# Kernel tuning notes

Measured on AMD Instinct MI355X. Metric: run time of the kernel, lower is better.

The kernel has to match this reference:

```python
import jax, jax.numpy as jnp
import numpy as np

B, N, DEG, RATIO = 100, 1000, 16, 0.8
E = B * N * DEG                      # 1.6M edges
K1 = int(np.ceil(RATIO * N))         # 800
K2 = int(np.ceil(RATIO * K1))        # 640
K3 = int(np.ceil(RATIO * K2))        # 512
F_IN, H, OUT = 128, 128, 10


def _graph_conv(x, src, dst, emask, w_root, w_rel, b):
    # PyG GraphConv (aggr='add'): out = lin_rel(sum_j x_j) + lin_root(x) + bias
    msg = x[src] * emask[:, None].astype(x.dtype)               # [E, F]
    agg = jax.ops.segment_sum(msg, dst, num_segments=x.shape[0])
    return agg @ w_rel.T + x @ w_root.T + b


def _topk_pool(x, src, dst, emask, w, n_per_graph, k):
    # PyG TopKPooling: score = tanh((x.w)/||w||); keep top-k per graph; x *= score
    score = jnp.tanh((x @ w) / jnp.linalg.norm(w))              # [B*n]
    vals, idx = jax.lax.top_k(score.reshape(B, n_per_graph), k)  # [B,k]
    perm = (idx + jnp.arange(B)[:, None] * n_per_graph).reshape(-1)
    new_x = x[perm] * vals.reshape(-1, 1)
    mapping = jnp.full(B * n_per_graph, -1, dtype=jnp.int32).at[perm].set(
        jnp.arange(B * k, dtype=jnp.int32))
    ns, nd = mapping[src], mapping[dst]
    valid = emask & (ns >= 0) & (nd >= 0)
    return new_x, jnp.where(valid, ns, 0), jnp.where(valid, nd, 0), valid


def _global_pool(x, k):
    xg = x.reshape(B, k, x.shape[-1])
    return jnp.concatenate([xg.max(axis=1), xg.mean(axis=1)], axis=1)  # [B, 2H]


def setup_inputs() -> dict:
    key = jax.random.key(0)
    ks = jax.random.split(key, 16)
    x = jax.random.normal(ks[0], (B * N, F_IN), jnp.float32)
    src = jax.random.randint(ks[1], (B, N * DEG), 0, N)
    dst = jax.random.randint(ks[2], (B, N * DEG), 0, N)
    off = (jnp.arange(B) * N)[:, None]
    edge_index = jnp.stack([(src + off).reshape(-1), (dst + off).reshape(-1)])

    def lin(k, fo, fi):
        return jax.random.normal(k, (fo, fi), jnp.float32) / np.sqrt(fi).astype(np.float32)

    return {
        'x': x, 'edge_index': edge_index,
        'w_root1': lin(ks[3], H, F_IN), 'w_rel1': lin(ks[4], H, F_IN), 'b1': jnp.zeros((H,), jnp.float32),
        'pw1': jax.random.normal(ks[5], (H,), jnp.float32),
        'w_root2': lin(ks[6], H, H), 'w_rel2': lin(ks[7], H, H), 'b2': jnp.zeros((H,), jnp.float32),
        'pw2': jax.random.normal(ks[8], (H,), jnp.float32),
        'w_root3': lin(ks[9], H, H), 'w_rel3': lin(ks[10], H, H), 'b3': jnp.zeros((H,), jnp.float32),
        'pw3': jax.random.normal(ks[11], (H,), jnp.float32),
        'lin1_w': lin(ks[12], 128, 256), 'lin1_b': jnp.zeros((128,), jnp.float32),
        'lin2_w': lin(ks[13], 64, 128), 'lin2_b': jnp.zeros((64,), jnp.float32),
        'lin3_w': lin(ks[14], OUT, 64), 'lin3_b': jnp.zeros((OUT,), jnp.float32),
    }


def reference(x, edge_index, w_root1, w_rel1, b1, pw1, w_root2, w_rel2, b2, pw2,
              w_root3, w_rel3, b3, pw3, lin1_w, lin1_b, lin2_w, lin2_b, lin3_w, lin3_b):
    src, dst = edge_index[0], edge_index[1]
    emask = jnp.ones(src.shape[0], dtype=bool)

    h = jax.nn.relu(_graph_conv(x, src, dst, emask, w_root1, w_rel1, b1))
    h, src, dst, emask = _topk_pool(h, src, dst, emask, pw1, N, K1)
    x1 = _global_pool(h, K1)

    h = jax.nn.relu(_graph_conv(h, src, dst, emask, w_root2, w_rel2, b2))
    h, src, dst, emask = _topk_pool(h, src, dst, emask, pw2, K1, K2)
    x2 = _global_pool(h, K2)

    h = jax.nn.relu(_graph_conv(h, src, dst, emask, w_root3, w_rel3, b3))
    h, src, dst, emask = _topk_pool(h, src, dst, emask, pw3, K2, K3)
    x3 = _global_pool(h, K3)

    g = x1 + x2 + x3                                   # [B, 256]
    g = jax.nn.relu(g @ lin1_w.T + lin1_b)             # dropout: eval mode (identity)
    g = jax.nn.relu(g @ lin2_w.T + lin2_b)
    return jax.nn.log_softmax(g @ lin3_w.T + lin3_b, axis=-1)
```

## Files before the change

kernel.cpp:

```cpp
#include <hip/hip_runtime.h>
#include <math.h>

constexpr int BG = 100;
constexpr int NN = 1000;
constexpr int EE = 1600000;
constexpr int NV = 100000;
constexpr int FD = 128;
constexpr int K1 = 800, K2 = 640, K3 = 512;

__device__ __forceinline__ float xla_tanh(float x) {
    const float kClamp = 7.90531110763549805f;
    const float a1 = 4.89352455891786e-03f, a3 = 6.37261928875436e-04f,
                a5 = 1.48572235717979e-05f, a7 = 5.12229709037114e-08f,
                a9 = -8.60467152213735e-11f, a11 = 2.00018790482477e-13f,
                a13 = -2.76076847742355e-16f;
    const float b0 = 4.89352518554385e-03f, b2 = 2.26843463243900e-03f,
                b4 = 1.18534705686654e-04f, b6 = 1.19825839466702e-06f;
    if (fabsf(x) < 4e-04f) return x;
    float xc = fminf(fmaxf(x, -kClamp), kClamp);
    float x2 = xc * xc;
    float p = fmaf(x2, a13, a11);
    p = fmaf(x2, p, a9);
    p = fmaf(x2, p, a7);
    p = fmaf(x2, p, a5);
    p = fmaf(x2, p, a3);
    p = fmaf(x2, p, a1);
    p = xc * p;
    float q = fmaf(x2, b6, b4);
    q = fmaf(x2, q, b2);
    q = fmaf(x2, q, b0);
    return p / q;
}

__global__ __launch_bounds__(256) void zero_k(int* __restrict__ p, int n) {
    int i = blockIdx.x * 256 + threadIdx.x;
    if (i < n) p[i] = 0;
}
__global__ __launch_bounds__(256) void count_k(const int* __restrict__ dst,
                                               int* __restrict__ cnt) {
    int e = blockIdx.x * 256 + threadIdx.x;
    if (e < EE) atomicAdd(&cnt[dst[e]], 1);
}
__global__ __launch_bounds__(1024) void scan1_k(const int* __restrict__ cnt,
                                                int* __restrict__ excl,
                                                int* __restrict__ bsum, int n) {
    __shared__ int s[1024];
    int b = blockIdx.x, t = threadIdx.x, i = b * 1024 + t;
    int v = (i < n) ? cnt[i] : 0;
    s[t] = v; __syncthreads();
    for (int off = 1; off < 1024; off <<= 1) {
        int x = (t >= off) ? s[t - off] : 0;
        __syncthreads();
        s[t] += x;
        __syncthreads();
    }
    if (i < n) excl[i] = s[t] - v;
    if (t == 1023) bsum[b] = s[t];
}
__global__ void scan2_k(int* __restrict__ bsum, int nb) {
    if (threadIdx.x == 0) {
        int acc = 0;
        for (int b = 0; b < nb; ++b) { int v = bsum[b]; bsum[b] = acc; acc += v; }
    }
}
__global__ __launch_bounds__(256) void scan3_k(int* __restrict__ rowptr,
                                               const int* __restrict__ bsum,
                                               int* __restrict__ cursor, int n) {
    int i = blockIdx.x * 256 + threadIdx.x;
    if (i < n) {
        int v = rowptr[i] + bsum[i >> 10];
        rowptr[i] = v;
        cursor[i] = v;
    }
    if (i == 0) rowptr[n] = EE;
}
__global__ __launch_bounds__(256) void fill_k(const int* __restrict__ dst,
                                              int* __restrict__ cursor,
                                              int* __restrict__ eidx) {
    int e = blockIdx.x * 256 + threadIdx.x;
    if (e < EE) {
        int p = atomicAdd(&cursor[dst[e]], 1);
        eidx[p] = e;
    }
}
__global__ __launch_bounds__(256) void compose_k(const int* __restrict__ m1,
                                                 const int* __restrict__ m2,
                                                 int* __restrict__ cm, int n) {
    int i = blockIdx.x * 256 + threadIdx.x;
    if (i < n) { int v = m1[i]; cm[i] = (v < 0) ? -1 : m2[v]; }
}

__global__ __launch_bounds__(128) void gather3_k(
    const float* __restrict__ feat, const int* __restrict__ src,
    const int* __restrict__ rowptr, const int* __restrict__ eidx,
    const int* __restrict__ map, float* __restrict__ agg)
{
    __shared__ int sS[128];
    __shared__ double sred[4][32][4];
    int bid = blockIdx.x;
    int d = (bid & 7) * (NV / 8) + (bid >> 3);
    int t = threadIdx.x;
    int slot = t >> 5;
    int fg   = t & 31;
    int dm = d;
    if (map) { dm = map[d]; if (dm < 0) return; }
    int beg = rowptr[d], end = rowptr[d + 1];
    double a0 = 0.0, a1 = 0.0, a2 = 0.0, a3 = 0.0;
    while (beg < end) {
        int chunk = min(128, end - beg);
        if (t < chunk) {
            int s = src[eidx[beg + t]];
            if (map) s = map[s];
            sS[t] = s;
        }
        __syncthreads();
        for (int i = slot; i < chunk; i += 4) {
            int s = sS[i];
            if (s >= 0) {
                float4 v = *(const float4*)(feat + (size_t)s * FD + fg * 4);
                a0 += (double)v.x; a1 += (double)v.y;
                a2 += (double)v.z; a3 += (double)v.w;
            }
        }
        __syncthreads();
        beg += chunk;
    }
    sred[slot][fg][0] = a0; sred[slot][fg][1] = a1;
    sred[slot][fg][2] = a2; sred[slot][fg][3] = a3;
    __syncthreads();
    if (slot == 0) {
        double r0 = sred[0][fg][0] + sred[1][fg][0] + sred[2][fg][0] + sred[3][fg][0];
        double r1 = sred[0][fg][1] + sred[1][fg][1] + sred[2][fg][1] + sred[3][fg][1];
        double r2 = sred[0][fg][2] + sred[1][fg][2] + sred[2][fg][2] + sred[3][fg][2];
        double r3 = sred[0][fg][3] + sred[1][fg][3] + sred[2][fg][3] + sred[3][fg][3];
        *(float4*)(agg + (size_t)dm * FD + fg * 4) =
            make_float4((float)r0, (float)r1, (float)r2, (float)r3);
    }
}

constexpr int TRR = 32;
constexpr int KS = 64;
constexpr int LDK2 = 68;
__global__ __launch_bounds__(128) void conv_mm4(
    const float* __restrict__ in, float* __restrict__ agg,
    const float* __restrict__ w_root, const float* __restrict__ w_rel,
    const float* __restrict__ bias)
{
    __shared__ float sA[TRR][LDK2];
    __shared__ float sI[TRR][LDK2];
    int r0 = blockIdx.x * TRR;
    int t = threadIdx.x;
    int g  = t >> 6;
    int cp = t & 63;
    const float* wr0 = w_rel  + (size_t)(2 * cp) * FD;
    const float* wr1 = wr0 + FD;
    const float* wo0 = w_root + (size_t)(2 * cp) * FD;
    const float* wo1 = wo0 + FD;
    float acc[2][16];
    #pragma unroll
    for (int c = 0; c < 2; ++c)
        #pragma unroll
        for (int r = 0; r < 16; ++r) acc[c][r] = 0.f;

    #pragma unroll
    for (int ph = 0; ph < 2; ++ph) {
        int kb = ph * KS;
        if (ph) __syncthreads();
        #pragma unroll
        for (int q = 0; q < 8; ++q) {
            int idx = q * 128 + t;
            int row = (idx >> 4) & 31;
            int c4  = idx & 15;
            if (idx < 512) {
                float4 va = *(const float4*)(agg + (size_t)(r0 + row) * FD + kb + c4 * 4);
                *(float4*)&sA[row][c4 * 4] = va;
            } else {
                float4 vi = *(const float4*)(in + (size_t)(r0 + row) * FD + kb + c4 * 4);
                *(float4*)&sI[row][c4 * 4] = vi;
            }
        }
        __syncthreads();
        for (int k0 = kb; k0 < kb + KS; k0 += 4) {
            float4 r0v = *(const float4*)(wr0 + k0);
            float4 r1v = *(const float4*)(wr1 + k0);
            float4 o0v = *(const float4*)(wo0 + k0);
            float4 o1v = *(const float4*)(wo1 + k0);
            int kl = k0 - kb;
            #pragma unroll
            for (int r = 0; r < 16; ++r) {
                float4 a = *(const float4*)&sA[g * 16 + r][kl];
                float4 b = *(const float4*)&sI[g * 16 + r][kl];
                acc[0][r] += a.x * r0v.x + b.x * o0v.x;
                acc[0][r] += a.y * r0v.y + b.y * o0v.y;
                acc[0][r] += a.z * r0v.z + b.z * o0v.z;
                acc[0][r] += a.w * r0v.w + b.w * o0v.w;
                acc[1][r] += a.x * r1v.x + b.x * o1v.x;
                acc[1][r] += a.y * r1v.y + b.y * o1v.y;
                acc[1][r] += a.z * r1v.z + b.z * o1v.z;
                acc[1][r] += a.w * r1v.w + b.w * o1v.w;
            }
        }
    }
    float b0 = bias[2 * cp], b1 = bias[2 * cp + 1];
    #pragma unroll
    for (int r = 0; r < 16; ++r) {
        float v0 = b0 + acc[0][r];
        float v1 = b1 + acc[1][r];
        v0 = v0 > 0.f ? v0 : 0.f;
        v1 = v1 > 0.f ? v1 : 0.f;
        *(float2*)(agg + (size_t)(r0 + g * 16 + r) * FD + 2 * cp) =
            make_float2(v0, v1);
    }
}

__global__ __launch_bounds__(128) void norm_k(const float* __restrict__ pw,
                                              float* __restrict__ nrm)
{
    int t = threadIdx.x;
    float v = pw[t]; v *= v;
    #pragma unroll
    for (int off = 32; off; off >>= 1) v += __shfl_down(v, off);
    __shared__ float s[2];
    if ((t & 63) == 0) s[t >> 6] = v;
    __syncthreads();
    if (t == 0) nrm[0] = sqrtf(s[0] + s[1]);
}

__global__ __launch_bounds__(256) void scores_k(
    const float* __restrict__ h, const float* __restrict__ pw,
    const float* __restrict__ nrm, float* __restrict__ out, int rows)
{
    int gid = blockIdx.x * 256 + threadIdx.x;
    int node = gid >> 6, lane = gid & 63;
    if (node >= rows) return;
    float2 hv = *(const float2*)(h + (size_t)node * FD + lane * 2);
    float2 wv = *(const float2*)(pw + lane * 2);
    double d = (double)hv.x * (double)wv.x + (double)hv.y * (double)wv.y;
    #pragma unroll
    for (int off = 32; off; off >>= 1) d += __shfl_down(d, off);
    if (lane == 0) {
        float arg = (float)d / nrm[0];
        out[node] = xla_tanh(arg);
    }
}

__global__ __launch_bounds__(512) void topk_k(
    const float* __restrict__ h, const float* __restrict__ scores,
    float* __restrict__ outx, int* __restrict__ mapping, int n_per, int k)
{
    __shared__ unsigned long long sk[1024];
    __shared__ int sel[1024];
    int b = blockIdx.x, tid = threadIdx.x;
    for (int i = tid; i < 1024; i += 512) {
        float f = (i < n_per) ? scores[b * n_per + i] : -INFINITY;
        unsigned u = __float_as_uint(f);
        u = (u & 0x80000000u) ? ~u : (u | 0x80000000u);
        sk[i] = ((unsigned long long)u << 32) | (unsigned)(1023 - i);
        sel[i] = -1;
    }
    __syncthreads();
    for (int ksz = 2; ksz <= 1024; ksz <<= 1) {
        for (int j = ksz >> 1; j; j >>= 1) {
            int i = ((tid & ~(j - 1)) << 1) | (tid & (j - 1));
            int p = i | j;
            bool up = ((i & ksz) == 0);
            unsigned long long ki = sk[i], kp = sk[p];
            if ((ki < kp) == up) { sk[i] = kp; sk[p] = ki; }
            __syncthreads();
        }
    }
    for (int i = tid; i < k; i += 512)
        sel[1023 - (unsigned)(sk[i] & 0xFFFFFFFFu)] = i;
    __syncthreads();
    for (int i = tid; i < n_per; i += 512)
        mapping[b * n_per + i] = (sel[i] >= 0) ? b * k + sel[i] : -1;
    for (int t = tid; t < k * 32; t += 512) {
        int nj = t >> 5, f4 = t & 31;
        unsigned long long kk = sk[nj];
        int old = 1023 - (unsigned)(kk & 0xFFFFFFFFu);
        unsigned u = (unsigned)(kk >> 32);
        float val = (u & 0x80000000u) ? __uint_as_float(u & 0x7FFFFFFFu)
                                      : __uint_as_float(~u);
        float4 v = *(const float4*)(h + (size_t)(b * n_per + old) * FD + f4 * 4);
        v.x *= val; v.y *= val; v.z *= val; v.w *= val;
        *(float4*)(outx + (size_t)(b * k + nj) * FD + f4 * 4) = v;
    }
}

__global__ __launch_bounds__(1024) void gpool2_k(const float* __restrict__ xp,
                                                 float* __restrict__ g, int k)
{
    __shared__ float smx[8][128];
    __shared__ float ssm[8][128];
    int b = blockIdx.x, t = threadIdx.x;
    int rg = t >> 7;
    int f  = t & 127;
    float mx = -INFINITY, sm = 0.f;
    for (int j = rg; j < k; j += 8) {
        float v = xp[(size_t)(b * k + j) * FD + f];
        mx = fmaxf(mx, v);
        sm += v;
    }
    smx[rg][f] = mx;
    ssm[rg][f] = sm;
    __syncthreads();
    if (rg == 0) {
        float m = smx[0][f], s = ssm[0][f];
        #pragma unroll
        for (int q = 1; q < 8; ++q) { m = fmaxf(m, smx[q][f]); s += ssm[q][f]; }
        g[b * 256 + f]       += m;
        g[b * 256 + 128 + f] += s * (1.0f / k);
    }
}

__global__ __launch_bounds__(256) void mlp_k(
    const float* __restrict__ g,
    const float* __restrict__ l1w, const float* __restrict__ l1b,
    const float* __restrict__ l2w, const float* __restrict__ l2b,
    const float* __restrict__ l3w, const float* __restrict__ l3b,
    float* __restrict__ out)
{
    __shared__ float s0[256], s1[128], s2[64], s3[10];
    int b = blockIdx.x, t = threadIdx.x;
    s0[t] = g[b * 256 + t];
    __syncthreads();
    if (t < 128) {
        float a = l1b[t];
        for (int kk = 0; kk < 256; ++kk) a += s0[kk] * l1w[t * 256 + kk];
        s1[t] = a > 0.f ? a : 0.f;
    }
    __syncthreads();
    if (t < 64) {
        float a = l2b[t];
        for (int kk = 0; kk < 128; ++kk) a += s1[kk] * l2w[t * 128 + kk];
        s2[t] = a > 0.f ? a : 0.f;
    }
    __syncthreads();
    if (t < 10) {
        float a = l3b[t];
        for (int kk = 0; kk < 64; ++kk) a += s2[kk] * l3w[t * 64 + kk];
        s3[t] = a;
    }
    __syncthreads();
    if (t == 0) {
        float m = s3[0];
        for (int i = 1; i < 10; ++i) m = fmaxf(m, s3[i]);
        float se = 0.f;
        for (int i = 0; i < 10; ++i) se += expf(s3[i] - m);
        float lse = m + logf(se);
        for (int i = 0; i < 10; ++i) out[b * 10 + i] = s3[i] - lse;
    }
}

extern "C" void kernel_launch(void* const* d_in, const int* in_sizes, int n_in,
                              void* d_out, int out_size, void* d_ws, size_t ws_size,
                              hipStream_t stream)
{
    const float* x       = (const float*)d_in[0];
    const int*   ei      = (const int*)d_in[1];
    const int*   src     = ei;
    const int*   dst     = ei + EE;
    const float* w_root1 = (const float*)d_in[2];
    const float* w_rel1  = (const float*)d_in[3];
    const float* b1      = (const float*)d_in[4];
    const float* pw1     = (const float*)d_in[5];
    const float* w_root2 = (const float*)d_in[6];
    const float* w_rel2  = (const float*)d_in[7];
    const float* b2      = (const float*)d_in[8];
    const float* pw2     = (const float*)d_in[9];
    const float* w_root3 = (const float*)d_in[10];
    const float* w_rel3  = (const float*)d_in[11];
    const float* b3      = (const float*)d_in[12];
    const float* pw3     = (const float*)d_in[13];
    const float* l1w     = (const float*)d_in[14];
    const float* l1b     = (const float*)d_in[15];
    const float* l2w     = (const float*)d_in[16];
    const float* l2b     = (const float*)d_in[17];
    const float* l3w     = (const float*)d_in[18];
    const float* l3b     = (const float*)d_in[19];
    float* out = (float*)d_out;

    float* A      = (float*)d_ws;
    float* Bf     = A + (size_t)NV * FD;
    float* scores = Bf + (size_t)80000 * FD;
    float* g      = scores + NV;
    float* nrm    = g + BG * 256;
    int*   map1   = (int*)(nrm + 64);
    int*   map2   = map1 + NV;
    int*   map3   = map2 + 80000;
    int*   rowptr = map3 + 64000;
    int*   cursor = rowptr + NV + 2;
    int*   bsum   = cursor + NV;
    int*   eidx   = bsum + 128;
    int*   cmap   = eidx + EE;

    const int NB_E = (EE + 255) / 256;
    const int NB_V = (NV + 255) / 256;
    const int NB_S = (NV + 1023) / 1024;

    zero_k<<<NB_V, 256, 0, stream>>>(cursor, NV);
    count_k<<<NB_E, 256, 0, stream>>>(dst, cursor);
    scan1_k<<<NB_S, 1024, 0, stream>>>(cursor, rowptr, bsum, NV);
    scan2_k<<<1, 64, 0, stream>>>(bsum, NB_S);
    scan3_k<<<NB_V, 256, 0, stream>>>(rowptr, bsum, cursor, NV);
    fill_k<<<NB_E, 256, 0, stream>>>(dst, cursor, eidx);

    hipMemsetAsync(g, 0, (size_t)BG * 256 * sizeof(float), stream);

    gather3_k<<<NV, 128, 0, stream>>>(x, src, rowptr, eidx, nullptr, A);
    conv_mm4<<<NV / TRR, 128, 0, stream>>>(x, A, w_root1, w_rel1, b1);
    norm_k<<<1, 128, 0, stream>>>(pw1, nrm);
    scores_k<<<NV / 4, 256, 0, stream>>>(A, pw1, nrm, scores, NV);
    topk_k<<<BG, 512, 0, stream>>>(A, scores, Bf, map1, NN, K1);
    gpool2_k<<<BG, 1024, 0, stream>>>(Bf, g, K1);

    gather3_k<<<NV, 128, 0, stream>>>(Bf, src, rowptr, eidx, map1, A);
    conv_mm4<<<(BG * K1) / TRR, 128, 0, stream>>>(Bf, A, w_root2, w_rel2, b2);
    norm_k<<<1, 128, 0, stream>>>(pw2, nrm);
    scores_k<<<(BG * K1) / 4, 256, 0, stream>>>(A, pw2, nrm, scores, BG * K1);
    topk_k<<<BG, 512, 0, stream>>>(A, scores, Bf, map2, K1, K2);
    gpool2_k<<<BG, 1024, 0, stream>>>(Bf, g, K2);

    compose_k<<<NB_V, 256, 0, stream>>>(map1, map2, cmap, NV);
    gather3_k<<<NV, 128, 0, stream>>>(Bf, src, rowptr, eidx, cmap, A);
    conv_mm4<<<(BG * K2) / TRR, 128, 0, stream>>>(Bf, A, w_root3, w_rel3, b3);
    norm_k<<<1, 128, 0, stream>>>(pw3, nrm);
    scores_k<<<(BG * K2) / 4, 256, 0, stream>>>(A, pw3, nrm, scores, BG * K2);
    topk_k<<<BG, 512, 0, stream>>>(A, scores, Bf, map3, K2, K3);
    gpool2_k<<<BG, 1024, 0, stream>>>(Bf, g, K3);

    mlp_k<<<BG, 256, 0, stream>>>(g, l1w, l1b, l2w, l2b, l3w, l3b, out);
}
```

Measured before the change: 922.6 us.

## Store source indices in CSR order and remap them in place per pooling level

```diff
diff --git a/kernel.cpp b/kernel.cpp
--- a/kernel.cpp
+++ b/kernel.cpp
@@ -75,13 +75,19 @@
     if (i == 0) rowptr[n] = EE;
 }
 __global__ __launch_bounds__(256) void fill_k(const int* __restrict__ dst,
+                                              const int* __restrict__ src,
                                               int* __restrict__ cursor,
-                                              int* __restrict__ eidx) {
+                                              int* __restrict__ msrc) {
     int e = blockIdx.x * 256 + threadIdx.x;
     if (e < EE) {
         int p = atomicAdd(&cursor[dst[e]], 1);
-        eidx[p] = e;
-    }
+        msrc[p] = src[e];
+    }
+}
+__global__ __launch_bounds__(256) void remap_k(const int* __restrict__ map,
+                                               int* __restrict__ msrc) {
+    int i = blockIdx.x * 256 + threadIdx.x;
+    if (i < EE) { int v = msrc[i]; msrc[i] = (v < 0) ? -1 : map[v]; }
 }
 __global__ __launch_bounds__(256) void compose_k(const int* __restrict__ m1,
                                                  const int* __restrict__ m2,
@@ -90,12 +96,11 @@
     if (i < n) { int v = m1[i]; cm[i] = (v < 0) ? -1 : m2[v]; }
 }
 
-__global__ __launch_bounds__(128) void gather3_k(
-    const float* __restrict__ feat, const int* __restrict__ src,
-    const int* __restrict__ rowptr, const int* __restrict__ eidx,
-    const int* __restrict__ map, float* __restrict__ agg)
-{
-    __shared__ int sS[128];
+__global__ __launch_bounds__(128) void gather5_k(
+    const float* __restrict__ feat, const int* __restrict__ rowptr,
+    const int* __restrict__ msrc, const int* __restrict__ map,
+    float* __restrict__ agg)
+{
     __shared__ double sred[4][32][4];
     int bid = blockIdx.x;
     int d = (bid & 7) * (NV / 8) + (bid >> 3);
@@ -106,24 +111,13 @@
     if (map) { dm = map[d]; if (dm < 0) return; }
     int beg = rowptr[d], end = rowptr[d + 1];
     double a0 = 0.0, a1 = 0.0, a2 = 0.0, a3 = 0.0;
-    while (beg < end) {
-        int chunk = min(128, end - beg);
-        if (t < chunk) {
-            int s = src[eidx[beg + t]];
-            if (map) s = map[s];
-            sS[t] = s;
+    for (int i = beg + slot; i < end; i += 4) {
+        int s = msrc[i];
+        if (s >= 0) {
+            float4 v = *(const float4*)(feat + (size_t)s * FD + fg * 4);
+            a0 += (double)v.x; a1 += (double)v.y;
+            a2 += (double)v.z; a3 += (double)v.w;
         }
-        __syncthreads();
-        for (int i = slot; i < chunk; i += 4) {
-            int s = sS[i];
-            if (s >= 0) {
-                float4 v = *(const float4*)(feat + (size_t)s * FD + fg * 4);
-                a0 += (double)v.x; a1 += (double)v.y;
-                a2 += (double)v.z; a3 += (double)v.w;
-            }
-        }
-        __syncthreads();
-        beg += chunk;
     }
     sred[slot][fg][0] = a0; sred[slot][fg][1] = a1;
     sred[slot][fg][2] = a2; sred[slot][fg][3] = a3;
@@ -391,8 +385,8 @@
     int*   rowptr = map3 + 64000;
     int*   cursor = rowptr + NV + 2;
     int*   bsum   = cursor + NV;
-    int*   eidx   = bsum + 128;
-    int*   cmap   = eidx + EE;
+    int*   msrc   = bsum + 128;
+    int*   cmap   = msrc + EE;
 
     const int NB_E = (EE + 255) / 256;
     const int NB_V = (NV + 255) / 256;
@@ -403,26 +397,28 @@
     scan1_k<<<NB_S, 1024, 0, stream>>>(cursor, rowptr, bsum, NV);
     scan2_k<<<1, 64, 0, stream>>>(bsum, NB_S);
     scan3_k<<<NB_V, 256, 0, stream>>>(rowptr, bsum, cursor, NV);
-    fill_k<<<NB_E, 256, 0, stream>>>(dst, cursor, eidx);
+    fill_k<<<NB_E, 256, 0, stream>>>(dst, src, cursor, msrc);
 
     hipMemsetAsync(g, 0, (size_t)BG * 256 * sizeof(float), stream);
 
-    gather3_k<<<NV, 128, 0, stream>>>(x, src, rowptr, eidx, nullptr, A);
+    gather5_k<<<NV, 128, 0, stream>>>(x, rowptr, msrc, nullptr, A);
     conv_mm4<<<NV / TRR, 128, 0, stream>>>(x, A, w_root1, w_rel1, b1);
     norm_k<<<1, 128, 0, stream>>>(pw1, nrm);
     scores_k<<<NV / 4, 256, 0, stream>>>(A, pw1, nrm, scores, NV);
     topk_k<<<BG, 512, 0, stream>>>(A, scores, Bf, map1, NN, K1);
     gpool2_k<<<BG, 1024, 0, stream>>>(Bf, g, K1);
 
-    gather3_k<<<NV, 128, 0, stream>>>(Bf, src, rowptr, eidx, map1, A);
+    remap_k<<<NB_E, 256, 0, stream>>>(map1, msrc);
+    gather5_k<<<NV, 128, 0, stream>>>(Bf, rowptr, msrc, map1, A);
     conv_mm4<<<(BG * K1) / TRR, 128, 0, stream>>>(Bf, A, w_root2, w_rel2, b2);
     norm_k<<<1, 128, 0, stream>>>(pw2, nrm);
     scores_k<<<(BG * K1) / 4, 256, 0, stream>>>(A, pw2, nrm, scores, BG * K1);
     topk_k<<<BG, 512, 0, stream>>>(A, scores, Bf, map2, K1, K2);
     gpool2_k<<<BG, 1024, 0, stream>>>(Bf, g, K2);
 
+    remap_k<<<NB_E, 256, 0, stream>>>(map2, msrc);
     compose_k<<<NB_V, 256, 0, stream>>>(map1, map2, cmap, NV);
-    gather3_k<<<NV, 128, 0, stream>>>(Bf, src, rowptr, eidx, cmap, A);
+    gather5_k<<<NV, 128, 0, stream>>>(Bf, rowptr, msrc, cmap, A);
     conv_mm4<<<(BG * K2) / TRR, 128, 0, stream>>>(Bf, A, w_root3, w_rel3, b3);
     norm_k<<<1, 128, 0, stream>>>(pw3, nrm);
     scores_k<<<(BG * K2) / 4, 256, 0, stream>>>(A, pw3, nrm, scores, BG * K2);
```

Result: no change. 940.6 us (+2.0%).
